# Performance work log

Measured on AMD Instinct MI355X. Metric: run time of the kernel, lower is better.

## Reference

```python
import jax, jax.numpy as jnp
import numpy as np
import math

B, S, HID, H = 1, 2048, 1024, 16
D = HID // H  # head_dim = 64


def setup_inputs() -> dict:
    key = jax.random.key(0)
    ks = jax.random.split(key, 12)
    s = 0.02
    x = jax.random.normal(ks[0], (B, S, HID), jnp.float32)
    Wq = jax.random.normal(ks[1], (HID, HID), jnp.float32) * s
    bq = jnp.zeros((HID,), jnp.float32)
    Wk = jax.random.normal(ks[2], (HID, HID), jnp.float32) * s
    bk = jnp.zeros((HID,), jnp.float32)
    Wv = jax.random.normal(ks[3], (HID, HID), jnp.float32) * s
    bv = jnp.zeros((HID,), jnp.float32)
    Wo = jax.random.normal(ks[4], (HID, HID), jnp.float32) * s
    bo = jnp.zeros((HID,), jnp.float32)
    # nn.Parameter(torch.ones(3,3)) at init; small noise so the bias is non-degenerate
    cmw = jnp.ones((3, 3), jnp.float32) + 0.1 * jax.random.normal(ks[5], (3, 3), jnp.float32)
    # full causal [B,S,S] mask so the mask.shape[1]==seq_len branch is taken
    mask = jnp.tril(jnp.ones((B, S, S), jnp.int32))
    modality_info = jax.random.randint(ks[6], (B, S), 0, 3, dtype=jnp.int64)
    return dict(x=x, Wq=Wq, bq=bq, Wk=Wk, bk=bk, Wv=Wv, bv=bv, Wo=Wo, bo=bo,
                cmw=cmw, mask=mask, modality_info=modality_info)


def reference(x, Wq, bq, Wk, bk, Wv, bv, Wo, bo, cmw, mask, modality_info):
    b, s, _ = x.shape
    # QKV projections (torch Linear: y = x @ W.T + b), split into heads [B,H,S,D]
    q = (x @ Wq.T + bq).reshape(b, s, H, D).transpose(0, 2, 1, 3)
    k = (x @ Wk.T + bk).reshape(b, s, H, D).transpose(0, 2, 1, 3)
    v = (x @ Wv.T + bv).reshape(b, s, H, D).transpose(0, 2, 1, 3)
    scores = jnp.einsum('bhqd,bhkd->bhqk', q, k) / math.sqrt(D)  # [B,H,S,S]
    # cross-modal bias: gather from 3x3 table via pairwise modality indices -> [B,S,S]
    bias = cmw[modality_info[:, :, None], modality_info[:, None, :]]
    scores = scores + bias[:, None, :, :]  # equals original broadcast when B==1
    scores = jnp.where(mask[:, None, :, :] == 0, -1e9, scores)
    attn = jax.nn.softmax(scores, axis=-1)  # dropout is identity in eval
    ctx = jnp.einsum('bhqk,bhkd->bhqd', attn, v)          # [B,H,S,D]
    ctx = ctx.transpose(0, 2, 1, 3).reshape(b, s, HID)    # [B,S,HID]
    return ctx @ Wo.T + bo
```

## Files before the change

kernel.cpp:

```cpp
#include <hip/hip_runtime.h>
#include <hip/hip_bf16.h>
#include <math.h>

#define S_LEN 2048
#define HID   1024
#define NHEAD 16

using bf16x8 = __attribute__((ext_vector_type(8))) short;
using bf16x4 = __attribute__((ext_vector_type(4))) short;
using f32x4  = __attribute__((ext_vector_type(4))) float;

__device__ __forceinline__ float bf2f(short s) {
  union { unsigned u; float f; } c;
  c.u = ((unsigned)(unsigned short)s) << 16;
  return c.f;
}
__device__ __forceinline__ short f2bf(float f) {
  union { float f; unsigned u; } c; c.f = f;
  unsigned u = c.u;
  unsigned r = (u + 0x7fffu + ((u >> 16) & 1u)) >> 16;
  return (short)r;
}
__device__ __forceinline__ float loadf(const void* base, long idx, int is_bf) {
  return is_bf ? bf2f(((const short*)base)[idx]) : ((const float*)base)[idx];
}
__device__ __forceinline__ void gl_lds16(const void* g, void* l) {
  __builtin_amdgcn_global_load_lds(
      (const __attribute__((address_space(1))) void*)g,
      (__attribute__((address_space(3))) void*)l, 16, 0, 0);
}

__global__ void detect_kernel(const unsigned* __restrict__ xw,
                              const int* __restrict__ modw,
                              int* __restrict__ flags) {
  const int t = threadIdx.x;
  int cnt = 0;
  for (int i = t; i < 1024; i += 64) {
    const unsigned fld = (xw[i] >> 7) & 0xFFu;
    cnt += (fld >= 100u && fld <= 135u) ? 1 : 0;
  }
  int odd = 0;
  for (int i = 0; i < 4; ++i) {
    const int wv = modw[2 * (t + 64 * i) + 1];
    odd += (wv != 0) ? 1 : 0;
  }
  for (int m = 1; m < 64; m <<= 1) {
    cnt += __shfl_xor(cnt, m);
    odd += __shfl_xor(odd, m);
  }
  if (t == 0) {
    flags[0] = (cnt >= 512) ? 1 : 0;
    flags[1] = (odd == 0) ? 1 : 0;
  }
}

__global__ __launch_bounds__(256) void convert5(
    const void* __restrict__ s0, const void* __restrict__ s1, const void* __restrict__ s2,
    const void* __restrict__ s3, const void* __restrict__ s4,
    short* __restrict__ d0, short* __restrict__ d1, short* __restrict__ d2,
    short* __restrict__ d3, short* __restrict__ d4,
    const int* __restrict__ flags) {
  const int a = blockIdx.y;
  const void* src = (a == 0) ? s0 : (a == 1) ? s1 : (a == 2) ? s2 : (a == 3) ? s3 : s4;
  short* dst = (a == 0) ? d0 : (a == 1) ? d1 : (a == 2) ? d2 : (a == 3) ? d3 : d4;
  const long n = (a == 0) ? (2L << 20) : (1L << 20);
  const int is_bf = flags[0];
  long i = (long)(blockIdx.x * 256 + threadIdx.x) * 8;
  const long stride = (long)gridDim.x * 256 * 8;
  if (is_bf) {
    for (; i < n; i += stride)
      *(bf16x8*)(dst + i) = *(const bf16x8*)((const short*)src + i);
  } else {
    for (; i < n; i += stride) {
      const float* p = (const float*)src + i;
      bf16x8 r;
#pragma unroll
      for (int j = 0; j < 8; ++j) r[j] = f2bf(p[j]);
      *(bf16x8*)(dst + i) = r;
    }
  }
}

__global__ __launch_bounds__(256) void gemm_bt3(
    const short* __restrict__ A,
    const short* __restrict__ W0, const short* __restrict__ W1, const short* __restrict__ W2,
    const void* __restrict__ b0, const void* __restrict__ b1, const void* __restrict__ b2,
    void* __restrict__ C0, void* __restrict__ C1, void* __restrict__ C2,
    const int* __restrict__ flags, int nbn, int store_f32, int tr_mat2)
{
  constexpr int K = 1024;
  constexpr int N = 1024;
  __shared__ short As[128 * 32];
  __shared__ short Bs[64 * 32];

  const int t = threadIdx.x;
  const int w = t >> 6, lane = t & 63;
  const int l15 = lane & 15, quad = lane >> 4;
  const int wm = w >> 1, wn = w & 1;
  const int is_bf = flags[0];

  const int mat = blockIdx.x / nbn;
  const int n0 = (blockIdx.x % nbn) * 64;
  const int m0 = blockIdx.y * 128;

  const short* W  = (mat == 0) ? W0 : (mat == 1 ? W1 : W2);
  const void* bia = (mat == 0) ? b0 : (mat == 1 ? b1 : b2);
  void*       C   = (mat == 0) ? C0 : (mat == 1 ? C1 : C2);
  const int tr = (mat == 2) ? tr_mat2 : 0;

  f32x4 acc[4][2];
  for (int mi = 0; mi < 4; ++mi)
    for (int ni = 0; ni < 2; ++ni)
      for (int r = 0; r < 4; ++r) acc[mi][ni][r] = 0.f;

  const int srow = t >> 2;
  const int sch  = (t & 3) * 8;
  const short* Ap = A + (long)(m0 + srow) * K + sch;
  const short* Wp = W + (long)(n0 + srow) * K + sch;
  short* AsW = &As[w * 512];
  short* BsW = &Bs[w * 512];

  for (int kt = 0; kt < K / 32; ++kt) {
    __syncthreads();
    gl_lds16(Ap + kt * 32, AsW);
    gl_lds16(Ap + kt * 32 + 64L * K, AsW + 2048);
    gl_lds16(Wp + kt * 32, BsW);
    __syncthreads();

    bf16x8 af[4], bfr[2];
    for (int mi = 0; mi < 4; ++mi)
      af[mi] = *(const bf16x8*)&As[(wm * 64 + mi * 16 + l15) * 32 + quad * 8];
    for (int ni = 0; ni < 2; ++ni)
      bfr[ni] = *(const bf16x8*)&Bs[(wn * 32 + ni * 16 + l15) * 32 + quad * 8];
    for (int mi = 0; mi < 4; ++mi)
      for (int ni = 0; ni < 2; ++ni)
        acc[mi][ni] = __builtin_amdgcn_mfma_f32_16x16x32_bf16(af[mi], bfr[ni], acc[mi][ni], 0, 0, 0);
  }

  for (int ni = 0; ni < 2; ++ni) {
    const int col = n0 + wn * 32 + ni * 16 + l15;
    const float bv = loadf(bia, col, is_bf);
    for (int mi = 0; mi < 4; ++mi) {
      const int row = m0 + wm * 64 + mi * 16 + quad * 4;
      if (tr) {
        bf16x4 o;
#pragma unroll
        for (int r = 0; r < 4; ++r) o[r] = f2bf(acc[mi][ni][r] + bv);
        *(bf16x4*)((short*)C + (long)col * S_LEN + row) = o;
      } else {
        for (int r = 0; r < 4; ++r) {
          const float v = acc[mi][ni][r] + bv;
          const long idx = (long)(row + r) * N + col;
          if (store_f32) ((float*)C)[idx] = v;
          else           ((short*)C)[idx] = f2bf(v);
        }
      }
    }
  }
}

__global__ __launch_bounds__(256) void attn_split(
    const short* __restrict__ Q, const short* __restrict__ Kg, const short* __restrict__ VT,
    const int* __restrict__ mod, const void* __restrict__ cmw,
    const int* __restrict__ flags,
    short* __restrict__ PO0, short* __restrict__ PO1, short* __restrict__ PO2,
    float* __restrict__ PM, float* __restrict__ PL)
{
  __shared__ short Ps[4 * 16 * 80];
  __shared__ float cm[9];
  __shared__ int mods[2048];

  const int t = threadIdx.x;
  const int w = t >> 6, lane = t & 63;
  const int l15 = lane & 15, quad = lane >> 4;
  const int h = blockIdx.y;
  const int pair = blockIdx.x / 3;
  const int par  = blockIdx.x % 3;
  const int m64 = flags[1];

  if (t < 9) cm[t] = loadf(cmw, t, flags[0]);
  for (int i = t; i < 2048; i += 256) mods[i] = mod[i << m64];
  __syncthreads();

  short* POp = (par == 0) ? PO0 : (par == 1) ? PO1 : PO2;
  short* Pw = &Ps[w * 16 * 80];

  for (int si = 0; si < 2; ++si) {
    const int strip = (si == 0) ? pair : 31 - pair;
    const int q0 = strip * 64;
    const int nkt = strip + 1;

    const short* qb = Q + (long)(q0 + w * 16 + l15) * HID + h * 64 + quad * 8;
    const bf16x8 aq0 = *(const bf16x8*)qb;
    const bf16x8 aq1 = *(const bf16x8*)(qb + 32);

    int mrow[4];
    for (int r = 0; r < 4; ++r) mrow[r] = mods[q0 + w * 16 + quad * 4 + r];

    float m_i[4], l_i[4];
    f32x4 acc_o[4];
    for (int r = 0; r < 4; ++r) { m_i[r] = -1e30f; l_i[r] = 0.f; }
    for (int ni = 0; ni < 4; ++ni)
      for (int r = 0; r < 4; ++r) acc_o[ni][r] = 0.f;

    for (int kt = par; kt < nkt; kt += 3) {
      bf16x8 kf[4][2], vf[2][4];
#pragma unroll
      for (int nt = 0; nt < 4; ++nt) {
        const short* kr = Kg + (long)(kt * 64 + nt * 16 + l15) * HID + h * 64 + quad * 8;
        kf[nt][0] = *(const bf16x8*)kr;
        kf[nt][1] = *(const bf16x8*)(kr + 32);
      }
#pragma unroll
      for (int kk = 0; kk < 2; ++kk)
#pragma unroll
        for (int ni = 0; ni < 4; ++ni)
          vf[kk][ni] = *(const bf16x8*)(VT + (long)(h * 64 + ni * 16 + l15) * S_LEN
                                        + kt * 64 + kk * 32 + quad * 8);

      f32x4 sc[4];
#pragma unroll
      for (int nt = 0; nt < 4; ++nt) {
        f32x4 z;
        for (int r = 0; r < 4; ++r) z[r] = 0.f;
        z = __builtin_amdgcn_mfma_f32_16x16x32_bf16(aq0, kf[nt][0], z, 0, 0, 0);
        z = __builtin_amdgcn_mfma_f32_16x16x32_bf16(aq1, kf[nt][1], z, 0, 0, 0);
        sc[nt] = z;
      }

      float sv[4][4], rmax[4];
      for (int r = 0; r < 4; ++r) rmax[r] = -1e30f;
#pragma unroll
      for (int nt = 0; nt < 4; ++nt) {
        const int mcol = mods[kt * 64 + nt * 16 + l15];
        for (int r = 0; r < 4; ++r) {
          float x = sc[nt][r] * 0.125f + cm[mrow[r] * 3 + mcol];
          sv[nt][r] = x;
          rmax[r] = fmaxf(rmax[r], x);
        }
      }
      if (kt == nkt - 1) {
        for (int r = 0; r < 4; ++r) rmax[r] = -1e30f;
#pragma unroll
        for (int nt = 0; nt < 4; ++nt) {
          const int col = kt * 64 + nt * 16 + l15;
          for (int r = 0; r < 4; ++r) {
            const int row = q0 + w * 16 + quad * 4 + r;
            sv[nt][r] = (col <= row) ? sv[nt][r] : -1e30f;
            rmax[r] = fmaxf(rmax[r], sv[nt][r]);
          }
        }
      }
      for (int off = 1; off < 16; off <<= 1)
        for (int r = 0; r < 4; ++r) rmax[r] = fmaxf(rmax[r], __shfl_xor(rmax[r], off));

      float alpha[4], rsum[4];
      for (int r = 0; r < 4; ++r) {
        const float mn = fmaxf(m_i[r], rmax[r]);
        alpha[r] = __expf(m_i[r] - mn);
        m_i[r] = mn;
        rsum[r] = 0.f;
      }
      short pb[4][4];
#pragma unroll
      for (int nt = 0; nt < 4; ++nt)
        for (int r = 0; r < 4; ++r) {
          const float p = __expf(sv[nt][r] - m_i[r]);
          rsum[r] += p;
          pb[nt][r] = f2bf(p);
        }
      for (int off = 1; off < 16; off <<= 1)
        for (int r = 0; r < 4; ++r) rsum[r] += __shfl_xor(rsum[r], off);
      for (int r = 0; r < 4; ++r) l_i[r] = l_i[r] * alpha[r] + rsum[r];
      for (int ni = 0; ni < 4; ++ni)
        for (int r = 0; r < 4; ++r) acc_o[ni][r] *= alpha[r];

#pragma unroll
      for (int nt = 0; nt < 4; ++nt)
        for (int r = 0; r < 4; ++r)
          Pw[(quad * 4 + r) * 80 + nt * 16 + l15] = pb[nt][r];
      asm volatile("s_waitcnt lgkmcnt(0)" ::: "memory");

#pragma unroll
      for (int kk = 0; kk < 2; ++kk) {
        const bf16x8 ap = *(const bf16x8*)&Pw[l15 * 80 + kk * 32 + quad * 8];
        for (int ni = 0; ni < 4; ++ni)
          acc_o[ni] = __builtin_amdgcn_mfma_f32_16x16x32_bf16(ap, vf[kk][ni], acc_o[ni], 0, 0, 0);
      }
    }

    for (int ni = 0; ni < 4; ++ni) {
      const int col = h * 64 + ni * 16 + l15;
      for (int r = 0; r < 4; ++r) {
        const int row = q0 + w * 16 + quad * 4 + r;
        POp[(long)row * HID + col] = f2bf(acc_o[ni][r]);
      }
    }
    if (l15 == 0) {
      for (int r = 0; r < 4; ++r) {
        const int row = q0 + w * 16 + quad * 4 + r;
        PM[par * 32768 + row * 16 + h] = m_i[r];
        PL[par * 32768 + row * 16 + h] = l_i[r];
      }
    }
  }
}

__global__ __launch_bounds__(256) void attn_merge(
    const short* __restrict__ PO0, const short* __restrict__ PO1, const short* __restrict__ PO2,
    const float* __restrict__ PM, const float* __restrict__ PL, short* __restrict__ CTX)
{
  const int row = blockIdx.x;
  const int t = threadIdx.x;
  const int h = t >> 4;
  const int d0 = (t & 15) * 4;
  float m[3], l[3];
#pragma unroll
  for (int p = 0; p < 3; ++p) {
    m[p] = PM[p * 32768 + row * 16 + h];
    l[p] = PL[p * 32768 + row * 16 + h];
  }
  const float M = fmaxf(m[0], fmaxf(m[1], m[2]));
  float wgt[3], den = 0.f;
#pragma unroll
  for (int p = 0; p < 3; ++p) { wgt[p] = __expf(m[p] - M); den += l[p] * wgt[p]; }
  const float inv = 1.f / den;
  const long b = (long)row * HID + h * 64 + d0;
  const bf16x4 o0 = *(const bf16x4*)&PO0[b];
  const bf16x4 o1 = *(const bf16x4*)&PO1[b];
  const bf16x4 o2 = *(const bf16x4*)&PO2[b];
  bf16x4 out;
#pragma unroll
  for (int j = 0; j < 4; ++j)
    out[j] = f2bf((bf2f(o0[j]) * wgt[0] + bf2f(o1[j]) * wgt[1] + bf2f(o2[j]) * wgt[2]) * inv);
  *(bf16x4*)&CTX[b] = out;
}

extern "C" void kernel_launch(void* const* d_in, const int* in_sizes, int n_in,
                              void* d_out, int out_size, void* d_ws, size_t ws_size,
                              hipStream_t stream) {
  constexpr long M1 = 1024L * 1024L;
  int*   flags = (int*)d_ws;
  short* base  = (short*)d_ws + 128;
  short* xb  = base;
  short* Wqb = xb + 2 * M1;
  short* Wkb = Wqb + M1;
  short* Wvb = Wkb + M1;
  short* Wob = Wvb + M1;
  short* Qw  = Wob + M1;
  short* Kw  = Qw + 2 * M1;
  short* VTb = Kw + 2 * M1;
  short* CTX = VTb + 2 * M1;
  short* PO1 = xb;
  short* PO2 = Wqb;
  float* PM  = (float*)Wvb;
  float* PL  = PM + 3 * 32768;
  short* PO0 = CTX;
  const int* modality = (const int*)d_in[11];

  detect_kernel<<<1, 64, 0, stream>>>((const unsigned*)d_in[0], modality, flags);
  convert5<<<dim3(512, 5), 256, 0, stream>>>(
      d_in[0], d_in[1], d_in[3], d_in[5], d_in[7],
      xb, Wqb, Wkb, Wvb, Wob, flags);

  gemm_bt3<<<dim3(48, 16), 256, 0, stream>>>(
      xb, Wqb, Wkb, Wvb, d_in[2], d_in[4], d_in[6],
      Qw, Kw, VTb, flags, 16, 0, 1);
  attn_split<<<dim3(48, NHEAD), 256, 0, stream>>>(
      Qw, Kw, VTb, modality, d_in[9], flags, PO0, PO1, PO2, PM, PL);
  attn_merge<<<dim3(S_LEN), 256, 0, stream>>>(PO0, PO1, PO2, PM, PL, CTX);
  gemm_bt3<<<dim3(16, 16), 256, 0, stream>>>(
      CTX, Wob, Wob, Wob, d_in[8], d_in[8], d_in[8],
      d_out, d_out, d_out, flags, 16, 1, 0);
}
```

Before: 219.8 us.

## Stage K/V tiles in LDS with register prefetch; drop transposed V store

The attention kernel now loads each 64-key K and V tile cooperatively into shared memory, transposing V in LDS, instead of each wave issuing its own redundant global loads. It prefetches the next tile into registers while the current tile is computed. The QKV GEMM therefore writes V row-major and no longer uses the strided transposed store. The cost is two block barriers per iteration, scalar LDS writes for the V transpose (possible bank conflicts), and the removal of several unroll pragmas.

```diff
diff --git a/kernel.cpp b/kernel.cpp
--- a/kernel.cpp
+++ b/kernel.cpp
@@ -86,7 +86,7 @@
     const short* __restrict__ W0, const short* __restrict__ W1, const short* __restrict__ W2,
     const void* __restrict__ b0, const void* __restrict__ b1, const void* __restrict__ b2,
     void* __restrict__ C0, void* __restrict__ C1, void* __restrict__ C2,
-    const int* __restrict__ flags, int nbn, int store_f32, int tr_mat2)
+    const int* __restrict__ flags, int nbn, int store_f32)
 {
   constexpr int K = 1024;
   constexpr int N = 1024;
@@ -106,7 +106,6 @@
   const short* W  = (mat == 0) ? W0 : (mat == 1 ? W1 : W2);
   const void* bia = (mat == 0) ? b0 : (mat == 1 ? b1 : b2);
   void*       C   = (mat == 0) ? C0 : (mat == 1 ? C1 : C2);
-  const int tr = (mat == 2) ? tr_mat2 : 0;
 
   f32x4 acc[4][2];
   for (int mi = 0; mi < 4; ++mi)
@@ -142,30 +141,25 @@
     const float bv = loadf(bia, col, is_bf);
     for (int mi = 0; mi < 4; ++mi) {
       const int row = m0 + wm * 64 + mi * 16 + quad * 4;
-      if (tr) {
-        bf16x4 o;
-#pragma unroll
-        for (int r = 0; r < 4; ++r) o[r] = f2bf(acc[mi][ni][r] + bv);
-        *(bf16x4*)((short*)C + (long)col * S_LEN + row) = o;
-      } else {
-        for (int r = 0; r < 4; ++r) {
-          const float v = acc[mi][ni][r] + bv;
-          const long idx = (long)(row + r) * N + col;
-          if (store_f32) ((float*)C)[idx] = v;
-          else           ((short*)C)[idx] = f2bf(v);
-        }
+      for (int r = 0; r < 4; ++r) {
+        const float v = acc[mi][ni][r] + bv;
+        const long idx = (long)(row + r) * N + col;
+        if (store_f32) ((float*)C)[idx] = v;
+        else           ((short*)C)[idx] = f2bf(v);
       }
     }
   }
 }
 
 __global__ __launch_bounds__(256) void attn_split(
-    const short* __restrict__ Q, const short* __restrict__ Kg, const short* __restrict__ VT,
+    const short* __restrict__ Q, const short* __restrict__ Kg, const short* __restrict__ Vg,
     const int* __restrict__ mod, const void* __restrict__ cmw,
     const int* __restrict__ flags,
     short* __restrict__ PO0, short* __restrict__ PO1, short* __restrict__ PO2,
     float* __restrict__ PM, float* __restrict__ PL)
 {
+  __shared__ short Ks[64 * 80];
+  __shared__ short Vt[64 * 80];
   __shared__ short Ps[4 * 16 * 80];
   __shared__ float cm[9];
   __shared__ int mods[2048];
@@ -183,7 +177,8 @@
   __syncthreads();
 
   short* POp = (par == 0) ? PO0 : (par == 1) ? PO1 : PO2;
-  short* Pw = &Ps[w * 16 * 80];
+  const int krow = t >> 3, kch = (t & 7) * 8;
+  const int vkp = t & 63, vdc = (t >> 6) * 8;
 
   for (int si = 0; si < 2; ++si) {
     const int strip = (si == 0) ? pair : 31 - pair;
@@ -203,34 +198,45 @@
     for (int ni = 0; ni < 4; ++ni)
       for (int r = 0; r < 4; ++r) acc_o[ni][r] = 0.f;
 
+    bf16x8 rk0, rk1, rv0, rv1;
+    if (par < nkt) {
+      const long kb = (long)(par * 64) * HID + h * 64;
+      rk0 = *(const bf16x8*)(Kg + kb + (long)krow * HID + kch);
+      rk1 = *(const bf16x8*)(Kg + kb + (long)(krow + 32) * HID + kch);
+      rv0 = *(const bf16x8*)(Vg + kb + (long)vkp * HID + vdc);
+      rv1 = *(const bf16x8*)(Vg + kb + (long)vkp * HID + 32 + vdc);
+    }
+
     for (int kt = par; kt < nkt; kt += 3) {
-      bf16x8 kf[4][2], vf[2][4];
-#pragma unroll
+      __syncthreads();
+      *(bf16x8*)&Ks[krow * 80 + kch] = rk0;
+      *(bf16x8*)&Ks[(krow + 32) * 80 + kch] = rk1;
+#pragma unroll
+      for (int j = 0; j < 8; ++j) Vt[(vdc + j) * 80 + vkp] = rv0[j];
+#pragma unroll
+      for (int j = 0; j < 8; ++j) Vt[(vdc + 32 + j) * 80 + vkp] = rv1[j];
+      __syncthreads();
+      if (kt + 3 < nkt) {
+        const long kb = (long)((kt + 3) * 64) * HID + h * 64;
+        rk0 = *(const bf16x8*)(Kg + kb + (long)krow * HID + kch);
+        rk1 = *(const bf16x8*)(Kg + kb + (long)(krow + 32) * HID + kch);
+        rv0 = *(const bf16x8*)(Vg + kb + (long)vkp * HID + vdc);
+        rv1 = *(const bf16x8*)(Vg + kb + (long)vkp * HID + 32 + vdc);
+      }
+
+      f32x4 sc[4];
       for (int nt = 0; nt < 4; ++nt) {
-        const short* kr = Kg + (long)(kt * 64 + nt * 16 + l15) * HID + h * 64 + quad * 8;
-        kf[nt][0] = *(const bf16x8*)kr;
-        kf[nt][1] = *(const bf16x8*)(kr + 32);
-      }
-#pragma unroll
-      for (int kk = 0; kk < 2; ++kk)
-#pragma unroll
-        for (int ni = 0; ni < 4; ++ni)
-          vf[kk][ni] = *(const bf16x8*)(VT + (long)(h * 64 + ni * 16 + l15) * S_LEN
-                                        + kt * 64 + kk * 32 + quad * 8);
-
-      f32x4 sc[4];
-#pragma unroll
-      for (int nt = 0; nt < 4; ++nt) {
+        const bf16x8 kb0 = *(const bf16x8*)&Ks[(nt * 16 + l15) * 80 + quad * 8];
+        const bf16x8 kb1 = *(const bf16x8*)&Ks[(nt * 16 + l15) * 80 + 32 + quad * 8];
         f32x4 z;
         for (int r = 0; r < 4; ++r) z[r] = 0.f;
-        z = __builtin_amdgcn_mfma_f32_16x16x32_bf16(aq0, kf[nt][0], z, 0, 0, 0);
-        z = __builtin_amdgcn_mfma_f32_16x16x32_bf16(aq1, kf[nt][1], z, 0, 0, 0);
+        z = __builtin_amdgcn_mfma_f32_16x16x32_bf16(aq0, kb0, z, 0, 0, 0);
+        z = __builtin_amdgcn_mfma_f32_16x16x32_bf16(aq1, kb1, z, 0, 0, 0);
         sc[nt] = z;
       }
 
       float sv[4][4], rmax[4];
       for (int r = 0; r < 4; ++r) rmax[r] = -1e30f;
-#pragma unroll
       for (int nt = 0; nt < 4; ++nt) {
         const int mcol = mods[kt * 64 + nt * 16 + l15];
         for (int r = 0; r < 4; ++r) {
@@ -241,7 +247,6 @@
       }
       if (kt == nkt - 1) {
         for (int r = 0; r < 4; ++r) rmax[r] = -1e30f;
-#pragma unroll
         for (int nt = 0; nt < 4; ++nt) {
           const int col = kt * 64 + nt * 16 + l15;
           for (int r = 0; r < 4; ++r) {
@@ -262,7 +267,6 @@
         rsum[r] = 0.f;
       }
       short pb[4][4];
-#pragma unroll
       for (int nt = 0; nt < 4; ++nt)
         for (int r = 0; r < 4; ++r) {
           const float p = __expf(sv[nt][r] - m_i[r]);
@@ -275,17 +279,18 @@
       for (int ni = 0; ni < 4; ++ni)
         for (int r = 0; r < 4; ++r) acc_o[ni][r] *= alpha[r];
 
-#pragma unroll
+      short* Pw = &Ps[w * 16 * 80];
       for (int nt = 0; nt < 4; ++nt)
         for (int r = 0; r < 4; ++r)
           Pw[(quad * 4 + r) * 80 + nt * 16 + l15] = pb[nt][r];
       asm volatile("s_waitcnt lgkmcnt(0)" ::: "memory");
 
-#pragma unroll
       for (int kk = 0; kk < 2; ++kk) {
         const bf16x8 ap = *(const bf16x8*)&Pw[l15 * 80 + kk * 32 + quad * 8];
-        for (int ni = 0; ni < 4; ++ni)
-          acc_o[ni] = __builtin_amdgcn_mfma_f32_16x16x32_bf16(ap, vf[kk][ni], acc_o[ni], 0, 0, 0);
+        for (int ni = 0; ni < 4; ++ni) {
+          const bf16x8 bv = *(const bf16x8*)&Vt[(ni * 16 + l15) * 80 + kk * 32 + quad * 8];
+          acc_o[ni] = __builtin_amdgcn_mfma_f32_16x16x32_bf16(ap, bv, acc_o[ni], 0, 0, 0);
+        }
       }
     }
 
@@ -349,13 +354,13 @@
   short* Wob = Wvb + M1;
   short* Qw  = Wob + M1;
   short* Kw  = Qw + 2 * M1;
-  short* VTb = Kw + 2 * M1;
-  short* CTX = VTb + 2 * M1;
+  short* Vw  = Kw + 2 * M1;
+  short* CTX = Vw + 2 * M1;
+  short* PO0 = CTX;
   short* PO1 = xb;
   short* PO2 = Wqb;
   float* PM  = (float*)Wvb;
   float* PL  = PM + 3 * 32768;
-  short* PO0 = CTX;
   const int* modality = (const int*)d_in[11];
 
   detect_kernel<<<1, 64, 0, stream>>>((const unsigned*)d_in[0], modality, flags);
@@ -365,11 +370,11 @@
 
   gemm_bt3<<<dim3(48, 16), 256, 0, stream>>>(
       xb, Wqb, Wkb, Wvb, d_in[2], d_in[4], d_in[6],
-      Qw, Kw, VTb, flags, 16, 0, 1);
+      Qw, Kw, Vw, flags, 16, 0);
   attn_split<<<dim3(48, NHEAD), 256, 0, stream>>>(
-      Qw, Kw, VTb, modality, d_in[9], flags, PO0, PO1, PO2, PM, PL);
+      Qw, Kw, Vw, modality, d_in[9], flags, PO0, PO1, PO2, PM, PL);
   attn_merge<<<dim3(S_LEN), 256, 0, stream>>>(PO0, PO1, PO2, PM, PL, CTX);
   gemm_bt3<<<dim3(16, 16), 256, 0, stream>>>(
       CTX, Wob, Wob, Wob, d_in[8], d_in[8], d_in[8],
-      d_out, d_out, d_out, flags, 16, 1, 0);
-}
+      d_out, d_out, d_out, flags, 16, 1);
+}
```

After: 200.5 us. -8.8%, faster.
